# Performance work log

Hardware: AMD Instinct MI355X
Metric: run time of the kernel (lower is better)

## Reference

```python
import jax, jax.numpy as jnp
import numpy as np

N = 100000   # points in input set
K = 1024     # num centroids AND max neighbors per ball (as in original code)
C = 64       # input feature channels
R = 0.2      # ball radius
LAYERS = (64, 64, 128)


def setup_inputs() -> dict:
    key = jax.random.key(0)
    ks = jax.random.split(key, 9)
    coords = jax.random.uniform(ks[0], (N, 3), dtype=jnp.float32)
    features = jax.random.normal(ks[1], (N, C), dtype=jnp.float32)
    centroid_idx = jax.random.randint(ks[2], (K,), 0, N)
    dims = (3 + C,) + LAYERS
    params = {}
    for i in range(len(LAYERS)):
        fin, fout = dims[i], dims[i + 1]
        params[f"W{i+1}"] = (jax.random.normal(ks[3 + i], (fin, fout), dtype=jnp.float32)
                             / np.float32(np.sqrt(fin)))
        params[f"b{i+1}"] = jax.random.normal(ks[6 + i], (fout,), dtype=jnp.float32) * 0.01
    return dict(coords=coords, features=features, centroid_idx=centroid_idx, **params)


def reference(coords, features, centroid_idx, W1, b1, W2, b2, W3, b3):
    cent = coords[centroid_idx]                                   # [K,3]
    # squared distances [K,N] without materializing [K,N,3]
    d2 = (jnp.sum(cent * cent, axis=-1)[:, None]
          + jnp.sum(coords * coords, axis=-1)[None, :]
          - 2.0 * cent @ coords.T)
    mask = d2 <= R * R                                            # ball query
    # take the FIRST K in-radius points in original index order (matches [:K])
    rank = jnp.cumsum(mask.astype(jnp.int32), axis=1) - 1
    sel = mask & (rank < K)
    order = jnp.where(sel, jnp.arange(N)[None, :], N)
    idx = jnp.sort(order, axis=1)[:, :K]                          # [K,K]
    valid = idx < N
    idx_c = jnp.minimum(idx, N - 1)
    rel = coords[idx_c] - cent[:, None, :]                        # centered coords
    x = jnp.concatenate([rel, features[idx_c]], axis=-1)          # [K,K,3+C]
    for W, b in ((W1, b1), (W2, b2), (W3, b3)):
        x = jax.nn.relu(x @ W + b)
    x = jnp.where(valid[:, :, None], x, -jnp.inf)
    new_features = jnp.max(x, axis=1)                             # per-region max pool
    return cent, new_features
```

## Files before the change

### kernel.cpp

```cpp
#include <hip/hip_runtime.h>
#include <hip/hip_bf16.h>

#define NPTS    100000
#define KCENT   1024
#define NSEG    391
#define NWORDS  1564
#define WSTRIDE 1600
#define MB_BLKS (NSEG*32)

typedef __attribute__((ext_vector_type(8))) short bf16x8;
typedef __attribute__((ext_vector_type(4))) float f32x4;
typedef unsigned long long u64;

__device__ __forceinline__ unsigned short f2bf(float x) {
  union { float f; unsigned u; } v; v.f = x;
  unsigned r = v.u + 0x7FFFu + ((v.u >> 16) & 1u);
  return (unsigned short)(r >> 16);
}
__device__ __forceinline__ unsigned pk2bf(float a, float b) {
  union { __hip_bfloat162 h; unsigned u; } cv;
  cv.h = __float22bfloat162_rn(make_float2(a, b));
  return cv.u;
}
__device__ __forceinline__ bf16x8 pack_bf8(f32x4 a, f32x4 b) {
  union { bf16x8 v; unsigned u[4]; } r;
  r.u[0] = pk2bf(a[0], a[1]); r.u[1] = pk2bf(a[2], a[3]);
  r.u[2] = pk2bf(b[0], b[1]); r.u[3] = pk2bf(b[2], b[3]);
  return r.v;
}

__global__ __launch_bounds__(256) void build_prep_kernel(
    const float* __restrict__ coords, const float* __restrict__ features,
    const int* __restrict__ cidx, const float* __restrict__ W1,
    const float* __restrict__ b1, const float* __restrict__ W2,
    const float* __restrict__ W3, u64* __restrict__ maskbuf,
    unsigned short* __restrict__ featsBF, f32x4* __restrict__ coords4,
    unsigned short* __restrict__ W1T, unsigned short* __restrict__ W2T,
    unsigned short* __restrict__ W3T, float* __restrict__ outCent) {
  const int bid = blockIdx.x;
  const int tid = threadIdx.x;
  if (bid < MB_BLKS) {
    const int grp = bid / NSEG, seg = bid - grp*NSEG;
    __shared__ float sC[96];
    __shared__ float sCC[32];
    if (tid < 96) sC[tid] = coords[cidx[grp*32 + tid/3]*3 + tid%3];
    __syncthreads();
    if (tid < 32) {
      float x = sC[tid*3], y = sC[tid*3+1], z = sC[tid*3+2];
      sCC[tid] = __fadd_rn(__fadd_rn(__fmul_rn(x,x), __fmul_rn(y,y)), __fmul_rn(z,z));
    }
    const int p = seg*256 + tid;
    const bool inr = p < NPTS;
    float px = 0.f, py = 0.f, pz = 0.f;
    if (inr) { px = coords[p*3]; py = coords[p*3+1]; pz = coords[p*3+2]; }
    const float pp = __fadd_rn(__fadd_rn(__fmul_rn(px,px), __fmul_rn(py,py)), __fmul_rn(pz,pz));
    __syncthreads();
    const int lane = tid & 63, wid = tid >> 6;
    u64 myw = 0ull;
    #pragma unroll
    for (int ci = 0; ci < 32; ++ci) {
      float cx = sC[ci*3], cy = sC[ci*3+1], cz = sC[ci*3+2];
      float dt = __fadd_rn(__fadd_rn(__fmul_rn(cx,px), __fmul_rn(cy,py)), __fmul_rn(cz,pz));
      float d2 = __fsub_rn(__fadd_rn(sCC[ci], pp), __fmul_rn(2.0f, dt));
      bool sel = inr && (d2 <= 0.04f);
      u64 m = __ballot(sel);
      if (lane == ci) myw = m;
    }
    if (lane < 32)
      maskbuf[(u64)(grp*32 + lane)*WSTRIDE + seg*4 + wid] = myw;
    return;
  }
  int i = (bid - MB_BLKS) * 256 + tid;
  if (i < 800000) {
    const f32x4* src = (const f32x4*)features + i*2;
    f32x4 f0 = src[0], f1 = src[1];
    union { bf16x8 v; uint4 u; } pk; pk.v = pack_bf8(f0, f1);
    ((uint4*)featsBF)[i] = pk.u;
    return;
  }
  i -= 800000;
  if (i < NPTS) {
    coords4[i] = (f32x4){coords[3*i], coords[3*i+1], coords[3*i+2], 0.f};
    return;
  }
  i -= NPTS;
  if (i < 6144) {
    int n = i / 96, kk = i - n*96;
    float v = 0.f;
    if (kk < 64)       v = W1[(3+kk)*64 + n];
    else if (kk < 67)  v = W1[(kk-64)*64 + n];
    else if (kk == 67) v = b1[n];
    W1T[n*96 + kk] = f2bf(v);
    return;
  }
  i -= 6144;
  if (i < 4608) { int n = i / 72, kk = i - n*72;
    W2T[n*72 + kk] = f2bf(kk < 64 ? W2[kk*64 + n] : 0.f); return; }
  i -= 4608;
  if (i < 9216) { int n = i / 72, kk = i - n*72;
    W3T[n*72 + kk] = f2bf(kk < 64 ? W3[kk*128 + n] : 0.f); return; }
  i -= 9216;
  if (i < KCENT) {
    int ci = cidx[i];
    outCent[i*3+0] = coords[ci*3+0];
    outCent[i*3+1] = coords[ci*3+1];
    outCent[i*3+2] = coords[ci*3+2];
  }
}

__global__ __launch_bounds__(256) void maskscan_kernel(
    const u64* __restrict__ maskbuf, int* __restrict__ idxbuf,
    int* __restrict__ counts) {
  const int tid = threadIdx.x;
  const int lane = tid & 63;
  const int c = blockIdx.x*4 + (tid >> 6);
  const u64* M = maskbuf + (u64)c * WSTRIDE;
  int* out = idxbuf + (c << 10);
  int base = 0;
  u64 word = (lane < NWORDS) ? M[lane] : 0ull;
  for (int chunk = 0; chunk < 25; ++chunk) {
    u64 next = 0ull;
    int wn = (chunk+1)*64 + lane;
    if (chunk+1 < 25 && wn < NWORDS) next = M[wn];
    int pc = __popcll(word);
    int inc = pc;
    #pragma unroll
    for (int d = 1; d < 64; d <<= 1) {
      int t = __shfl_up(inc, d);
      if (lane >= d) inc += t;
    }
    int tot = __shfl(inc, 63);
    int pos = base + inc - pc;
    while (word != 0ull && pos < KCENT) {
      int b = __ffsll((unsigned long long)word) - 1;
      out[pos++] = chunk*4096 + lane*64 + b;
      word &= word - 1ull;
    }
    base += tot;
    if (base >= KCENT) break;
    word = next;
  }
  if (lane == 0) counts[c] = base < KCENT ? base : KCENT;
}

__global__ __launch_bounds__(256, 2) void fused_kernel(
    const unsigned short* __restrict__ featsBF, const f32x4* __restrict__ coords4,
    const float* __restrict__ cent, const int* __restrict__ idxbuf,
    const int* __restrict__ counts, const float* __restrict__ b2v,
    const unsigned short* __restrict__ gW1T, const unsigned short* __restrict__ gW2T,
    const unsigned short* __restrict__ gW3T, float* __restrict__ pmax) {
  __shared__ __align__(16) unsigned short sW2T[64*72];
  __shared__ __align__(16) unsigned short sH[4*2*16*72];
  __shared__ float sB2[64];
  __shared__ float sMax[512];

  const int bx = blockIdx.x;
  const int k = bx >> 1, b = bx & 1;
  const int tid = threadIdx.x;
  const int w = tid >> 6, lane = tid & 63;
  const int q = lane >> 4, cl = lane & 15;

  for (int i = tid; i < 576; i += 256) ((uint4*)sW2T)[i] = ((const uint4*)gW2T)[i];
  if (tid < 64) sB2[tid] = b2v[tid];

  bf16x8 w1f[3][4], w3f[2][8];
  #pragma unroll
  for (int ks = 0; ks < 3; ++ks)
    #pragma unroll
    for (int nt = 0; nt < 4; ++nt)
      w1f[ks][nt] = *(const bf16x8*)(gW1T + (nt*16+cl)*96 + ks*32 + q*8);
  #pragma unroll
  for (int ks = 0; ks < 2; ++ks)
    #pragma unroll
    for (int nt = 0; nt < 8; ++nt)
      w3f[ks][nt] = *(const bf16x8*)(gW3T + (nt*16+cl)*72 + ks*32 + q*8);

  const int count = counts[k];
  const float cx = cent[k*3], cy = cent[k*3+1], cz = cent[k*3+2];
  unsigned short* myHA = sH + w*2304;
  unsigned short* myHB = myHA + 1152;
  const int kb = k << 10;
  __syncthreads();

  f32x4 runmax[8];
  #pragma unroll
  for (int i = 0; i < 8; ++i)
    runmax[i] = (f32x4){-__builtin_inff(), -__builtin_inff(),
                        -__builtin_inff(), -__builtin_inff()};

  const int nstrips = (count + 15) >> 4;
  const int npairs  = (nstrips + 1) >> 1;
  int pp = 2*w + b;

  int pA = 0, pB = 0;
  { int jA = 32*pp + cl;      if (jA < count) pA = idxbuf[kb + jA];
    int jB = 32*pp + 16 + cl; if (jB < count) pB = idxbuf[kb + jB]; }
  f32x4  c4A = coords4[pA], c4B = coords4[pB];
  bf16x8 xfA0 = *(const bf16x8*)(featsBF + pA*64 + q*8);
  bf16x8 xfA1 = *(const bf16x8*)(featsBF + pA*64 + 32 + q*8);
  bf16x8 xfB0 = *(const bf16x8*)(featsBF + pB*64 + q*8);
  bf16x8 xfB1 = *(const bf16x8*)(featsBF + pB*64 + 32 + q*8);
  int pA2 = 0, pB2 = 0;
  { int jA = 32*(pp+8) + cl;      if (jA < count) pA2 = idxbuf[kb + jA];
    int jB = 32*(pp+8) + 16 + cl; if (jB < count) pB2 = idxbuf[kb + jB]; }

  const bf16x8 zero8 = (bf16x8){0,0,0,0,0,0,0,0};

  for (; pp < npairs; pp += 8) {
    int pA3 = 0, pB3 = 0;
    { int jA = 32*(pp+16) + cl;      if (jA < count) pA3 = idxbuf[kb + jA];
      int jB = 32*(pp+16) + 16 + cl; if (jB < count) pB3 = idxbuf[kb + jB]; }
    f32x4  c4An = coords4[pA2], c4Bn = coords4[pB2];
    bf16x8 xfA0n = *(const bf16x8*)(featsBF + pA2*64 + q*8);
    bf16x8 xfA1n = *(const bf16x8*)(featsBF + pA2*64 + 32 + q*8);
    bf16x8 xfB0n = *(const bf16x8*)(featsBF + pB2*64 + q*8);
    bf16x8 xfB1n = *(const bf16x8*)(featsBF + pB2*64 + 32 + q*8);

    union { bf16x8 v; unsigned u[4]; } rfA, rfB;
    rfA.u[0] = pk2bf(c4A[0]-cx, c4A[1]-cy); rfA.u[1] = pk2bf(c4A[2]-cz, 1.0f);
    rfA.u[2] = 0u; rfA.u[3] = 0u;
    rfB.u[0] = pk2bf(c4B[0]-cx, c4B[1]-cy); rfB.u[1] = pk2bf(c4B[2]-cz, 1.0f);
    rfB.u[2] = 0u; rfB.u[3] = 0u;
    bf16x8 x2A = (q == 0) ? rfA.v : zero8;
    bf16x8 x2B = (q == 0) ? rfB.v : zero8;

    {
      f32x4 accA[4], accB[4];
      #pragma unroll
      for (int nt = 0; nt < 4; ++nt) { accA[nt] = (f32x4){0.f,0.f,0.f,0.f};
                                       accB[nt] = (f32x4){0.f,0.f,0.f,0.f}; }
      #pragma unroll
      for (int nt = 0; nt < 4; ++nt) {
        accA[nt] = __builtin_amdgcn_mfma_f32_16x16x32_bf16(w1f[0][nt], xfA0, accA[nt], 0,0,0);
        accB[nt] = __builtin_amdgcn_mfma_f32_16x16x32_bf16(w1f[0][nt], xfB0, accB[nt], 0,0,0);
      }
      #pragma unroll
      for (int nt = 0; nt < 4; ++nt) {
        accA[nt] = __builtin_amdgcn_mfma_f32_16x16x32_bf16(w1f[1][nt], xfA1, accA[nt], 0,0,0);
        accB[nt] = __builtin_amdgcn_mfma_f32_16x16x32_bf16(w1f[1][nt], xfB1, accB[nt], 0,0,0);
      }
      #pragma unroll
      for (int nt = 0; nt < 4; ++nt) {
        accA[nt] = __builtin_amdgcn_mfma_f32_16x16x32_bf16(w1f[2][nt], x2A, accA[nt], 0,0,0);
        accB[nt] = __builtin_amdgcn_mfma_f32_16x16x32_bf16(w1f[2][nt], x2B, accB[nt], 0,0,0);
      }
      #pragma unroll
      for (int nt = 0; nt < 4; ++nt) {
        const int o = nt*16 + q*4;
        uint2 pkA = { pk2bf(fmaxf(accA[nt][0],0.f), fmaxf(accA[nt][1],0.f)),
                      pk2bf(fmaxf(accA[nt][2],0.f), fmaxf(accA[nt][3],0.f)) };
        *(uint2*)(myHA + cl*72 + o) = pkA;
        uint2 pkB = { pk2bf(fmaxf(accB[nt][0],0.f), fmaxf(accB[nt][1],0.f)),
                      pk2bf(fmaxf(accB[nt][2],0.f), fmaxf(accB[nt][3],0.f)) };
        *(uint2*)(myHB + cl*72 + o) = pkB;
      }
    }

    {
      bf16x8 w2r[2][4];
      #pragma unroll
      for (int ks = 0; ks < 2; ++ks)
        #pragma unroll
        for (int nt = 0; nt < 4; ++nt)
          w2r[ks][nt] = *(const bf16x8*)(sW2T + (nt*16+cl)*72 + ks*32 + q*8);
      bf16x8 hA0 = *(const bf16x8*)(myHA + cl*72 + q*8);
      bf16x8 hA1 = *(const bf16x8*)(myHA + cl*72 + 32 + q*8);
      bf16x8 hB0 = *(const bf16x8*)(myHB + cl*72 + q*8);
      bf16x8 hB1 = *(const bf16x8*)(myHB + cl*72 + 32 + q*8);
      f32x4 accA[4], accB[4];
      #pragma unroll
      for (int nt = 0; nt < 4; ++nt) { accA[nt] = (f32x4){0.f,0.f,0.f,0.f};
                                       accB[nt] = (f32x4){0.f,0.f,0.f,0.f}; }
      #pragma unroll
      for (int nt = 0; nt < 4; ++nt) {
        accA[nt] = __builtin_amdgcn_mfma_f32_16x16x32_bf16(w2r[0][nt], hA0, accA[nt], 0,0,0);
        accB[nt] = __builtin_amdgcn_mfma_f32_16x16x32_bf16(w2r[0][nt], hB0, accB[nt], 0,0,0);
      }
      #pragma unroll
      for (int nt = 0; nt < 4; ++nt) {
        accA[nt] = __builtin_amdgcn_mfma_f32_16x16x32_bf16(w2r[1][nt], hA1, accA[nt], 0,0,0);
        accB[nt] = __builtin_amdgcn_mfma_f32_16x16x32_bf16(w2r[1][nt], hB1, accB[nt], 0,0,0);
      }
      #pragma unroll
      for (int nt = 0; nt < 4; ++nt) {
        const int o = nt*16 + q*4;
        f32x4 bb = *(const f32x4*)(sB2 + o);
        uint2 pkA = { pk2bf(fmaxf(accA[nt][0]+bb[0],0.f), fmaxf(accA[nt][1]+bb[1],0.f)),
                      pk2bf(fmaxf(accA[nt][2]+bb[2],0.f), fmaxf(accA[nt][3]+bb[3],0.f)) };
        *(uint2*)(myHA + cl*72 + o) = pkA;
        uint2 pkB = { pk2bf(fmaxf(accB[nt][0]+bb[0],0.f), fmaxf(accB[nt][1]+bb[1],0.f)),
                      pk2bf(fmaxf(accB[nt][2]+bb[2],0.f), fmaxf(accB[nt][3]+bb[3],0.f)) };
        *(uint2*)(myHB + cl*72 + o) = pkB;
      }
    }

    const float vmA = (32*pp + cl      < count) ? 0.f : -__builtin_inff();
    const float vmB = (32*pp + 16 + cl < count) ? 0.f : -__builtin_inff();
    {
      bf16x8 hA0 = *(const bf16x8*)(myHA + cl*72 + q*8);
      bf16x8 hA1 = *(const bf16x8*)(myHA + cl*72 + 32 + q*8);
      f32x4 acc3[8];
      #pragma unroll
      for (int nt = 0; nt < 8; ++nt) acc3[nt] = (f32x4){0.f,0.f,0.f,0.f};
      #pragma unroll
      for (int nt = 0; nt < 8; ++nt)
        acc3[nt] = __builtin_amdgcn_mfma_f32_16x16x32_bf16(w3f[0][nt], hA0, acc3[nt], 0,0,0);
      #pragma unroll
      for (int nt = 0; nt < 8; ++nt)
        acc3[nt] = __builtin_amdgcn_mfma_f32_16x16x32_bf16(w3f[1][nt], hA1, acc3[nt], 0,0,0);
      #pragma unroll
      for (int nt = 0; nt < 8; ++nt)
        #pragma unroll
        for (int r = 0; r < 4; ++r)
          runmax[nt][r] = fmaxf(runmax[nt][r], acc3[nt][r] + vmA);
    }
    {
      bf16x8 hB0 = *(const bf16x8*)(myHB + cl*72 + q*8);
      bf16x8 hB1 = *(const bf16x8*)(myHB + cl*72 + 32 + q*8);
      f32x4 acc3[8];
      #pragma unroll
      for (int nt = 0; nt < 8; ++nt) acc3[nt] = (f32x4){0.f,0.f,0.f,0.f};
      #pragma unroll
      for (int nt = 0; nt < 8; ++nt)
        acc3[nt] = __builtin_amdgcn_mfma_f32_16x16x32_bf16(w3f[0][nt], hB0, acc3[nt], 0,0,0);
      #pragma unroll
      for (int nt = 0; nt < 8; ++nt)
        acc3[nt] = __builtin_amdgcn_mfma_f32_16x16x32_bf16(w3f[1][nt], hB1, acc3[nt], 0,0,0);
      #pragma unroll
      for (int nt = 0; nt < 8; ++nt)
        #pragma unroll
        for (int r = 0; r < 4; ++r)
          runmax[nt][r] = fmaxf(runmax[nt][r], acc3[nt][r] + vmB);
    }

    c4A = c4An; c4B = c4Bn;
    xfA0 = xfA0n; xfA1 = xfA1n; xfB0 = xfB0n; xfB1 = xfB1n;
    pA2 = pA3; pB2 = pB3;
  }

  #pragma unroll
  for (int nt = 0; nt < 8; ++nt) {
    #pragma unroll
    for (int r = 0; r < 4; ++r) {
      float m = runmax[nt][r];
      m = fmaxf(m, __shfl_xor(m, 1));
      m = fmaxf(m, __shfl_xor(m, 2));
      m = fmaxf(m, __shfl_xor(m, 4));
      m = fmaxf(m, __shfl_xor(m, 8));
      runmax[nt][r] = m;
    }
    if (cl == 0) *(f32x4*)(sMax + w*128 + nt*16 + q*4) = runmax[nt];
  }
  __syncthreads();
  if (tid < 128) {
    float m = fmaxf(fmaxf(sMax[tid], sMax[128+tid]),
                    fmaxf(sMax[256+tid], sMax[384+tid]));
    pmax[bx*128 + tid] = m;
  }
}

__global__ __launch_bounds__(256) void combine_kernel(
    const float* __restrict__ pmax, const float* __restrict__ b3,
    float* __restrict__ outF) {
  int i = blockIdx.x*256 + threadIdx.x;
  int kk = i >> 7, c = i & 127;
  float m = fmaxf(pmax[(2*kk)*128 + c], pmax[(2*kk+1)*128 + c]);
  outF[i] = fmaxf(m + b3[c], 0.f);
}

extern "C" void kernel_launch(void* const* d_in, const int* in_sizes, int n_in,
                              void* d_out, int out_size, void* d_ws, size_t ws_size,
                              hipStream_t stream) {
  const float* coords   = (const float*)d_in[0];
  const float* features = (const float*)d_in[1];
  const int*   cidx     = (const int*)d_in[2];
  const float* W1 = (const float*)d_in[3];
  const float* b1 = (const float*)d_in[4];
  const float* W2 = (const float*)d_in[5];
  const float* b2 = (const float*)d_in[6];
  const float* W3 = (const float*)d_in[7];
  const float* b3 = (const float*)d_in[8];
  float* out = (float*)d_out;

  char* ws = (char*)d_ws;
  u64* maskbuf            = (u64*)(ws + 0);
  unsigned short* featsBF = (unsigned short*)(ws + 13107200);
  f32x4* coords4          = (f32x4*)(ws + 25907200);
  int* idxbuf  = (int*)(ws + 27507200);
  int* counts  = (int*)(ws + 31701504);
  unsigned short* W1T = (unsigned short*)(ws + 31705600);
  unsigned short* W2T = (unsigned short*)(ws + 31717888);
  unsigned short* W3T = (unsigned short*)(ws + 31727104);
  float* pmax = (float*)(ws + 31745536);

  build_prep_kernel<<<MB_BLKS + 3598, 256, 0, stream>>>(
      coords, features, cidx, W1, b1, W2, W3,
      maskbuf, featsBF, coords4, W1T, W2T, W3T, out);
  maskscan_kernel<<<256, 256, 0, stream>>>(maskbuf, idxbuf, counts);
  fused_kernel<<<2048, 256, 0, stream>>>(featsBF, coords4, out, idxbuf, counts,
                                         b2, W1T, W2T, W3T, pmax);
  combine_kernel<<<512, 256, 0, stream>>>(pmax, b3, out + 3072);
}
```

Baseline: 239.9 us.

## Stage MLP weights in LDS to raise occupancy; scan masks with block per centroid

```diff
diff --git a/kernel.cpp b/kernel.cpp
--- a/kernel.cpp
+++ b/kernel.cpp
@@ -90,7 +90,7 @@
     if (kk < 64)       v = W1[(3+kk)*64 + n];
     else if (kk < 67)  v = W1[(kk-64)*64 + n];
     else if (kk == 67) v = b1[n];
-    W1T[n*96 + kk] = f2bf(v);
+    W1T[n*104 + kk] = f2bf(v);
     return;
   }
   i -= 6144;
@@ -108,20 +108,25 @@
   }
 }
 
-__global__ __launch_bounds__(256) void maskscan_kernel(
+__global__ __launch_bounds__(256) void maskemit_kernel(
     const u64* __restrict__ maskbuf, int* __restrict__ idxbuf,
     int* __restrict__ counts) {
+  __shared__ int sTot[4];
+  const int c = blockIdx.x;
   const int tid = threadIdx.x;
-  const int lane = tid & 63;
-  const int c = blockIdx.x*4 + (tid >> 6);
+  const int lane = tid & 63, w = tid >> 6;
   const u64* M = maskbuf + (u64)c * WSTRIDE;
   int* out = idxbuf + (c << 10);
+  u64 wv[7];
+  #pragma unroll
+  for (int r = 0; r < 7; ++r) {
+    int widx = r*256 + tid;
+    wv[r] = (widx < NWORDS) ? M[widx] : 0ull;
+  }
   int base = 0;
-  u64 word = (lane < NWORDS) ? M[lane] : 0ull;
-  for (int chunk = 0; chunk < 25; ++chunk) {
-    u64 next = 0ull;
-    int wn = (chunk+1)*64 + lane;
-    if (chunk+1 < 25 && wn < NWORDS) next = M[wn];
+  #pragma unroll 1
+  for (int r = 0; r < 7; ++r) {
+    u64 word = wv[r];
     int pc = __popcll(word);
     int inc = pc;
     #pragma unroll
@@ -129,27 +134,34 @@
       int t = __shfl_up(inc, d);
       if (lane >= d) inc += t;
     }
-    int tot = __shfl(inc, 63);
-    int pos = base + inc - pc;
+    if (lane == 63) sTot[w] = inc;
+    __syncthreads();
+    int wbase = 0, tot = 0;
+    #pragma unroll
+    for (int i = 0; i < 4; ++i) { int v = sTot[i]; tot += v; if (i < w) wbase += v; }
+    int pos = base + wbase + inc - pc;
+    const int pbase = (r*256 + tid) * 64;
     while (word != 0ull && pos < KCENT) {
-      int b = __ffsll((unsigned long long)word) - 1;
-      out[pos++] = chunk*4096 + lane*64 + b;
+      int b = __ffsll(word) - 1;
+      out[pos++] = pbase + b;
       word &= word - 1ull;
     }
     base += tot;
+    __syncthreads();
     if (base >= KCENT) break;
-    word = next;
-  }
-  if (lane == 0) counts[c] = base < KCENT ? base : KCENT;
-}
-
-__global__ __launch_bounds__(256, 2) void fused_kernel(
+  }
+  if (tid == 0) counts[c] = base < KCENT ? base : KCENT;
+}
+
+__global__ __launch_bounds__(256, 3) void fused_kernel(
     const unsigned short* __restrict__ featsBF, const f32x4* __restrict__ coords4,
     const float* __restrict__ cent, const int* __restrict__ idxbuf,
     const int* __restrict__ counts, const float* __restrict__ b2v,
     const unsigned short* __restrict__ gW1T, const unsigned short* __restrict__ gW2T,
     const unsigned short* __restrict__ gW3T, float* __restrict__ pmax) {
+  __shared__ __align__(16) unsigned short sW1T[64*104];
   __shared__ __align__(16) unsigned short sW2T[64*72];
+  __shared__ __align__(16) unsigned short sW3T[128*72];
   __shared__ __align__(16) unsigned short sH[4*2*16*72];
   __shared__ float sB2[64];
   __shared__ float sMax[512];
@@ -160,20 +172,10 @@
   const int w = tid >> 6, lane = tid & 63;
   const int q = lane >> 4, cl = lane & 15;
 
-  for (int i = tid; i < 576; i += 256) ((uint4*)sW2T)[i] = ((const uint4*)gW2T)[i];
+  for (int i = tid; i < 832; i += 256)  ((uint4*)sW1T)[i] = ((const uint4*)gW1T)[i];
+  for (int i = tid; i < 576; i += 256)  ((uint4*)sW2T)[i] = ((const uint4*)gW2T)[i];
+  for (int i = tid; i < 1152; i += 256) ((uint4*)sW3T)[i] = ((const uint4*)gW3T)[i];
   if (tid < 64) sB2[tid] = b2v[tid];
-
-  bf16x8 w1f[3][4], w3f[2][8];
-  #pragma unroll
-  for (int ks = 0; ks < 3; ++ks)
-    #pragma unroll
-    for (int nt = 0; nt < 4; ++nt)
-      w1f[ks][nt] = *(const bf16x8*)(gW1T + (nt*16+cl)*96 + ks*32 + q*8);
-  #pragma unroll
-  for (int ks = 0; ks < 2; ++ks)
-    #pragma unroll
-    for (int nt = 0; nt < 8; ++nt)
-      w3f[ks][nt] = *(const bf16x8*)(gW3T + (nt*16+cl)*72 + ks*32 + q*8);
 
   const int count = counts[k];
   const float cx = cent[k*3], cy = cent[k*3+1], cz = cent[k*3+2];
@@ -210,11 +212,6 @@
     int pA3 = 0, pB3 = 0;
     { int jA = 32*(pp+16) + cl;      if (jA < count) pA3 = idxbuf[kb + jA];
       int jB = 32*(pp+16) + 16 + cl; if (jB < count) pB3 = idxbuf[kb + jB]; }
-    f32x4  c4An = coords4[pA2], c4Bn = coords4[pB2];
-    bf16x8 xfA0n = *(const bf16x8*)(featsBF + pA2*64 + q*8);
-    bf16x8 xfA1n = *(const bf16x8*)(featsBF + pA2*64 + 32 + q*8);
-    bf16x8 xfB0n = *(const bf16x8*)(featsBF + pB2*64 + q*8);
-    bf16x8 xfB1n = *(const bf16x8*)(featsBF + pB2*64 + 32 + q*8);
 
     union { bf16x8 v; unsigned u[4]; } rfA, rfB;
     rfA.u[0] = pk2bf(c4A[0]-cx, c4A[1]-cy); rfA.u[1] = pk2bf(c4A[2]-cz, 1.0f);
@@ -231,18 +228,16 @@
                                        accB[nt] = (f32x4){0.f,0.f,0.f,0.f}; }
       #pragma unroll
       for (int nt = 0; nt < 4; ++nt) {
-        accA[nt] = __builtin_amdgcn_mfma_f32_16x16x32_bf16(w1f[0][nt], xfA0, accA[nt], 0,0,0);
-        accB[nt] = __builtin_amdgcn_mfma_f32_16x16x32_bf16(w1f[0][nt], xfB0, accB[nt], 0,0,0);
-      }
-      #pragma unroll
-      for (int nt = 0; nt < 4; ++nt) {
-        accA[nt] = __builtin_amdgcn_mfma_f32_16x16x32_bf16(w1f[1][nt], xfA1, accA[nt], 0,0,0);
-        accB[nt] = __builtin_amdgcn_mfma_f32_16x16x32_bf16(w1f[1][nt], xfB1, accB[nt], 0,0,0);
-      }
-      #pragma unroll
-      for (int nt = 0; nt < 4; ++nt) {
-        accA[nt] = __builtin_amdgcn_mfma_f32_16x16x32_bf16(w1f[2][nt], x2A, accA[nt], 0,0,0);
-        accB[nt] = __builtin_amdgcn_mfma_f32_16x16x32_bf16(w1f[2][nt], x2B, accB[nt], 0,0,0);
+        const unsigned short* wrow = sW1T + (nt*16+cl)*104 + q*8;
+        bf16x8 wa0 = *(const bf16x8*)(wrow);
+        accA[nt] = __builtin_amdgcn_mfma_f32_16x16x32_bf16(wa0, xfA0, accA[nt], 0,0,0);
+        accB[nt] = __builtin_amdgcn_mfma_f32_16x16x32_bf16(wa0, xfB0, accB[nt], 0,0,0);
+        bf16x8 wa1 = *(const bf16x8*)(wrow + 32);
+        accA[nt] = __builtin_amdgcn_mfma_f32_16x16x32_bf16(wa1, xfA1, accA[nt], 0,0,0);
+        accB[nt] = __builtin_amdgcn_mfma_f32_16x16x32_bf16(wa1, xfB1, accB[nt], 0,0,0);
+        bf16x8 wa2 = *(const bf16x8*)(wrow + 64);
+        accA[nt] = __builtin_amdgcn_mfma_f32_16x16x32_bf16(wa2, x2A, accA[nt], 0,0,0);
+        accB[nt] = __builtin_amdgcn_mfma_f32_16x16x32_bf16(wa2, x2B, accB[nt], 0,0,0);
       }
       #pragma unroll
       for (int nt = 0; nt < 4; ++nt) {
@@ -256,13 +251,13 @@
       }
     }
 
+    c4A = coords4[pA2]; c4B = coords4[pB2];
+    xfA0 = *(const bf16x8*)(featsBF + pA2*64 + q*8);
+    xfA1 = *(const bf16x8*)(featsBF + pA2*64 + 32 + q*8);
+    xfB0 = *(const bf16x8*)(featsBF + pB2*64 + q*8);
+    xfB1 = *(const bf16x8*)(featsBF + pB2*64 + 32 + q*8);
+
     {
-      bf16x8 w2r[2][4];
-      #pragma unroll
-      for (int ks = 0; ks < 2; ++ks)
-        #pragma unroll
-        for (int nt = 0; nt < 4; ++nt)
-          w2r[ks][nt] = *(const bf16x8*)(sW2T + (nt*16+cl)*72 + ks*32 + q*8);
       bf16x8 hA0 = *(const bf16x8*)(myHA + cl*72 + q*8);
       bf16x8 hA1 = *(const bf16x8*)(myHA + cl*72 + 32 + q*8);
       bf16x8 hB0 = *(const bf16x8*)(myHB + cl*72 + q*8);
@@ -273,13 +268,13 @@
                                        accB[nt] = (f32x4){0.f,0.f,0.f,0.f}; }
       #pragma unroll
       for (int nt = 0; nt < 4; ++nt) {
-        accA[nt] = __builtin_amdgcn_mfma_f32_16x16x32_bf16(w2r[0][nt], hA0, accA[nt], 0,0,0);
-        accB[nt] = __builtin_amdgcn_mfma_f32_16x16x32_bf16(w2r[0][nt], hB0, accB[nt], 0,0,0);
-      }
-      #pragma unroll
-      for (int nt = 0; nt < 4; ++nt) {
-        accA[nt] = __builtin_amdgcn_mfma_f32_16x16x32_bf16(w2r[1][nt], hA1, accA[nt], 0,0,0);
-        accB[nt] = __builtin_amdgcn_mfma_f32_16x16x32_bf16(w2r[1][nt], hB1, accB[nt], 0,0,0);
+        const unsigned short* wrow = sW2T + (nt*16+cl)*72 + q*8;
+        bf16x8 wa0 = *(const bf16x8*)(wrow);
+        accA[nt] = __builtin_amdgcn_mfma_f32_16x16x32_bf16(wa0, hA0, accA[nt], 0,0,0);
+        accB[nt] = __builtin_amdgcn_mfma_f32_16x16x32_bf16(wa0, hB0, accB[nt], 0,0,0);
+        bf16x8 wa1 = *(const bf16x8*)(wrow + 32);
+        accA[nt] = __builtin_amdgcn_mfma_f32_16x16x32_bf16(wa1, hA1, accA[nt], 0,0,0);
+        accB[nt] = __builtin_amdgcn_mfma_f32_16x16x32_bf16(wa1, hB1, accB[nt], 0,0,0);
       }
       #pragma unroll
       for (int nt = 0; nt < 4; ++nt) {
@@ -294,47 +289,41 @@
       }
     }
 
-    const float vmA = (32*pp + cl      < count) ? 0.f : -__builtin_inff();
-    const float vmB = (32*pp + 16 + cl < count) ? 0.f : -__builtin_inff();
     {
       bf16x8 hA0 = *(const bf16x8*)(myHA + cl*72 + q*8);
       bf16x8 hA1 = *(const bf16x8*)(myHA + cl*72 + 32 + q*8);
-      f32x4 acc3[8];
-      #pragma unroll
-      for (int nt = 0; nt < 8; ++nt) acc3[nt] = (f32x4){0.f,0.f,0.f,0.f};
-      #pragma unroll
-      for (int nt = 0; nt < 8; ++nt)
-        acc3[nt] = __builtin_amdgcn_mfma_f32_16x16x32_bf16(w3f[0][nt], hA0, acc3[nt], 0,0,0);
-      #pragma unroll
-      for (int nt = 0; nt < 8; ++nt)
-        acc3[nt] = __builtin_amdgcn_mfma_f32_16x16x32_bf16(w3f[1][nt], hA1, acc3[nt], 0,0,0);
-      #pragma unroll
-      for (int nt = 0; nt < 8; ++nt)
-        #pragma unroll
-        for (int r = 0; r < 4; ++r)
-          runmax[nt][r] = fmaxf(runmax[nt][r], acc3[nt][r] + vmA);
-    }
-    {
       bf16x8 hB0 = *(const bf16x8*)(myHB + cl*72 + q*8);
       bf16x8 hB1 = *(const bf16x8*)(myHB + cl*72 + 32 + q*8);
-      f32x4 acc3[8];
-      #pragma unroll
-      for (int nt = 0; nt < 8; ++nt) acc3[nt] = (f32x4){0.f,0.f,0.f,0.f};
-      #pragma unroll
-      for (int nt = 0; nt < 8; ++nt)
-        acc3[nt] = __builtin_amdgcn_mfma_f32_16x16x32_bf16(w3f[0][nt], hB0, acc3[nt], 0,0,0);
-      #pragma unroll
-      for (int nt = 0; nt < 8; ++nt)
-        acc3[nt] = __builtin_amdgcn_mfma_f32_16x16x32_bf16(w3f[1][nt], hB1, acc3[nt], 0,0,0);
-      #pragma unroll
-      for (int nt = 0; nt < 8; ++nt)
+      const float vmA = (32*pp + cl      < count) ? 0.f : -__builtin_inff();
+      const float vmB = (32*pp + 16 + cl < count) ? 0.f : -__builtin_inff();
+      #pragma unroll
+      for (int ntq = 0; ntq < 4; ++ntq) {
+        f32x4 a3A[2], a3B[2];
         #pragma unroll
-        for (int r = 0; r < 4; ++r)
-          runmax[nt][r] = fmaxf(runmax[nt][r], acc3[nt][r] + vmB);
-    }
-
-    c4A = c4An; c4B = c4Bn;
-    xfA0 = xfA0n; xfA1 = xfA1n; xfB0 = xfB0n; xfB1 = xfB1n;
+        for (int j = 0; j < 2; ++j) { a3A[j] = (f32x4){0.f,0.f,0.f,0.f};
+                                      a3B[j] = (f32x4){0.f,0.f,0.f,0.f}; }
+        #pragma unroll
+        for (int j = 0; j < 2; ++j) {
+          const int nt = ntq*2 + j;
+          const unsigned short* wrow = sW3T + (nt*16+cl)*72 + q*8;
+          bf16x8 w30 = *(const bf16x8*)(wrow);
+          a3A[j] = __builtin_amdgcn_mfma_f32_16x16x32_bf16(w30, hA0, a3A[j], 0,0,0);
+          a3B[j] = __builtin_amdgcn_mfma_f32_16x16x32_bf16(w30, hB0, a3B[j], 0,0,0);
+          bf16x8 w31 = *(const bf16x8*)(wrow + 32);
+          a3A[j] = __builtin_amdgcn_mfma_f32_16x16x32_bf16(w31, hA1, a3A[j], 0,0,0);
+          a3B[j] = __builtin_amdgcn_mfma_f32_16x16x32_bf16(w31, hB1, a3B[j], 0,0,0);
+        }
+        #pragma unroll
+        for (int j = 0; j < 2; ++j) {
+          const int nt = ntq*2 + j;
+          #pragma unroll
+          for (int r = 0; r < 4; ++r)
+            runmax[nt][r] = fmaxf(runmax[nt][r],
+                                  fmaxf(a3A[j][r] + vmA, a3B[j][r] + vmB));
+        }
+      }
+    }
+
     pA2 = pA3; pB2 = pB3;
   }
 
@@ -389,14 +378,14 @@
   int* idxbuf  = (int*)(ws + 27507200);
   int* counts  = (int*)(ws + 31701504);
   unsigned short* W1T = (unsigned short*)(ws + 31705600);
-  unsigned short* W2T = (unsigned short*)(ws + 31717888);
-  unsigned short* W3T = (unsigned short*)(ws + 31727104);
-  float* pmax = (float*)(ws + 31745536);
+  unsigned short* W2T = (unsigned short*)(ws + 31718912);
+  unsigned short* W3T = (unsigned short*)(ws + 31728128);
+  float* pmax = (float*)(ws + 31746560);
 
   build_prep_kernel<<<MB_BLKS + 3598, 256, 0, stream>>>(
       coords, features, cidx, W1, b1, W2, W3,
       maskbuf, featsBF, coords4, W1T, W2T, W3T, out);
-  maskscan_kernel<<<256, 256, 0, stream>>>(maskbuf, idxbuf, counts);
+  maskemit_kernel<<<KCENT, 256, 0, stream>>>(maskbuf, idxbuf, counts);
   fused_kernel<<<2048, 256, 0, stream>>>(featsBF, coords4, out, idxbuf, counts,
                                          b2, W1T, W2T, W3T, pmax);
   combine_kernel<<<512, 256, 0, stream>>>(pmax, b3, out + 3072);
```

Result: no change. 243.6 us (+1.6%).
